# Performance work log

Measured on AMD Instinct MI355X. Metric: run time of the kernel, lower is better.

## Reference

```python
import jax, jax.numpy as jnp
import numpy as np

D_MODEL = 128
NHEAD = 8
DFF = 256
NW = 1024      # number of windows
WIN = 128      # max tokens per window
N_TOTAL = NW * WIN
NEG = -1e9


def _build_indices():
    rng = np.random.RandomState(0)
    cnt = rng.randint(WIN // 2, WIN + 1, size=NW)
    cnt_prv = rng.randint(WIN // 2, WIN + 1, size=NW)
    inds = np.concatenate([w * WIN + np.arange(c) for w, c in enumerate(cnt)]).astype(np.int64)
    inds_prv = np.concatenate([w * WIN + np.arange(c) for w, c in enumerate(cnt_prv)]).astype(np.int64)
    kpm_prv = (np.arange(WIN)[None, :] >= cnt_prv[:, None])  # True = padded key slot
    keep_inds = np.sort(rng.choice(N_TOTAL, len(inds), replace=False)).astype(np.int64)
    keep_inds_prv = np.sort(rng.choice(N_TOTAL, len(inds_prv), replace=False)).astype(np.int64)
    return inds, inds_prv, kpm_prv, keep_inds, keep_inds_prv


def setup_inputs() -> dict:
    inds, inds_prv, kpm_prv, keep_inds, keep_inds_prv = _build_indices()
    key = jax.random.key(0)
    ks = jax.random.split(key, 12)
    f = jnp.float32
    s = 0.05
    d, dff = D_MODEL, DFF
    return {
        'src': jax.random.normal(ks[0], (N_TOTAL, d), f),
        'src_prv': jax.random.normal(ks[1], (N_TOTAL, d), f),
        'pos': jax.random.normal(ks[2], (NW, WIN, d), f),
        'pos_prv': jax.random.normal(ks[3], (NW, WIN, d), f),
        'in_proj_w': jax.random.normal(ks[4], (3 * d, d), f) * s,
        'in_proj_b': jnp.zeros((3 * d,), f),
        'out_proj_w': jax.random.normal(ks[5], (d, d), f) * s,
        'out_proj_b': jnp.zeros((d,), f),
        'lin1_w': jax.random.normal(ks[6], (dff, d), f) * s,
        'lin1_b': jnp.zeros((dff,), f),
        'lin2_w': jax.random.normal(ks[7], (d, dff), f) * s,
        'lin2_b': jnp.zeros((d,), f),
        'ln1_g': jnp.ones((d,), f),
        'ln1_b': jnp.zeros((d,), f),
        'ln2_g': jnp.ones((d,), f),
        'ln2_b': jnp.zeros((d,), f),
        'keep_inds': jnp.asarray(keep_inds),
        'keep_inds_prv': jnp.asarray(keep_inds_prv),
        'inds': jnp.asarray(inds),
        'inds_prv': jnp.asarray(inds_prv),
        'key_padding_mask_prv': jnp.asarray(kpm_prv),
    }


def _layer_norm(x, g, b, eps=1e-5):
    m = x.mean(-1, keepdims=True)
    v = ((x - m) ** 2).mean(-1, keepdims=True)
    return (x - m) / jnp.sqrt(v + eps) * g + b


def reference(src, src_prv, pos, pos_prv, in_proj_w, in_proj_b, out_proj_w, out_proj_b,
              lin1_w, lin1_b, lin2_w, lin2_b, ln1_g, ln1_b, ln2_g, ln2_b,
              keep_inds, keep_inds_prv, inds, inds_prv, key_padding_mask_prv):
    d, h = D_MODEL, NHEAD
    hd = d // h
    # src[keep_inds] gather, then flat2window_v2 scatter into window grid
    sel = src[keep_inds]
    sel_prv = src_prv[keep_inds_prv]
    grid = jnp.zeros((NW * WIN, d), src.dtype).at[inds].set(sel).reshape(NW, WIN, d)
    grid_prv = jnp.zeros((NW * WIN, d), src.dtype).at[inds_prv].set(sel_prv).reshape(NW, WIN, d)
    q = grid + pos
    k = grid_prv + pos_prv
    v = grid_prv
    wq, wk, wv = jnp.split(in_proj_w, 3, axis=0)
    bq, bk, bv = jnp.split(in_proj_b, 3, axis=0)
    qh = (q @ wq.T + bq).reshape(NW, WIN, h, hd)
    kh = (k @ wk.T + bk).reshape(NW, WIN, h, hd)
    vh = (v @ wv.T + bv).reshape(NW, WIN, h, hd)
    scores = jnp.einsum('nqhd,nkhd->nhqk', qh, kh) / np.sqrt(hd).astype(np.float32)
    scores = jnp.where(key_padding_mask_prv[:, None, None, :], NEG, scores)
    attn = jax.nn.softmax(scores, axis=-1)
    out = jnp.einsum('nhqk,nkhd->nqhd', attn, vh).reshape(NW, WIN, d)
    out = out @ out_proj_w.T + out_proj_b
    # window2flat_v2 gather back, residual add at kept positions
    out_sel = out.reshape(NW * WIN, d)[inds]
    src = src.at[keep_inds].add(out_sel)  # dropout1 is identity in eval
    src = _layer_norm(src, ln1_g, ln1_b)
    ff = jax.nn.relu(src @ lin1_w.T + lin1_b) @ lin2_w.T + lin2_b
    src = _layer_norm(src + ff, ln2_g, ln2_b)
    return src
```

## Files before the change

kernel.cpp:

```cpp
#include <hip/hip_runtime.h>

#define NWIN 1024
#define WIN 128
#define DM 128
#define NTOT (NWIN*WIN)

typedef __bf16 bf16;
typedef __bf16 bf16x2 __attribute__((ext_vector_type(2)));
typedef __bf16 bf16x4 __attribute__((ext_vector_type(4)));
typedef __bf16 bf16x8 __attribute__((ext_vector_type(8)));
typedef float f32x4 __attribute__((ext_vector_type(4)));
typedef float f32x16 __attribute__((ext_vector_type(16)));

#define MFMA16(a,b,c) __builtin_amdgcn_mfma_f32_16x16x32_bf16(a,b,c,0,0,0)
#define MFMA32(a,b,c) __builtin_amdgcn_mfma_f32_32x32x16_bf16(a,b,c,0,0,0)

#define QSCALE 0.36067376022224085f


__global__ void k_prep1(const float* __restrict__ inproj, const float* __restrict__ outproj,
                        const float* __restrict__ w1, const float* __restrict__ w2,
                        bf16* __restrict__ whi,
                        int* __restrict__ mq, int* __restrict__ mkv, int* __restrict__ flag) {
    int i = blockIdx.x * 256 + threadIdx.x;
    if (i == 0) *flag = 0;
    float v;
    if (i < 49152)       v = inproj[i];
    else if (i < 65536)  v = outproj[i - 49152];
    else if (i < 98304)  v = w1[i - 65536];
    else                 v = w2[i - 98304];
    if (i < 16384) v *= QSCALE;
    whi[i] = (bf16)v;
    mq[i] = -1; mkv[i] = -1;
}

__global__ void k_prep2(const int* __restrict__ kpm_i, int* __restrict__ flag,
                        const int* __restrict__ inds, const int* __restrict__ keep, int n,
                        const int* __restrict__ inds_p, const int* __restrict__ keep_p, int np,
                        int* __restrict__ mq, int* __restrict__ mkv) {
    int j = blockIdx.x * 256 + threadIdx.x;
    if (j < 32768) {
        int v = kpm_i[j];
        if (v != 0 && v != 1) atomicOr(flag, 1);
    }
    if (j < n)  mq[inds[j]]    = keep[j];
    if (j < np) mkv[inds_p[j]] = keep_p[j];
}

__global__ void k_prep3(const int* __restrict__ kpm_i, const unsigned char* __restrict__ kpm_b,
                        const int* __restrict__ flag, unsigned char* __restrict__ kmask,
                        const float4* __restrict__ s, float4* __restrict__ d, int n4) {
    int i = blockIdx.x * 256 + threadIdx.x;
    if (i < 131072) {
        int byte_mode = *flag;
        kmask[i] = byte_mode ? (kpm_b[i] != 0) : (kpm_i[i] != 0);
    }
    int stride = gridDim.x * 256;
    for (int k = i; k < n4; k += stride) d[k] = s[k];
}

__device__ __forceinline__ void proj1p(const bf16* __restrict__ Xh,
                                       const bf16* __restrict__ WH,
                                       int l15, int g16, f32x4 acc[8]) {
    #pragma unroll
    for (int ks = 0; ks < 4; ks++) {
        bf16x8 ah = *(const bf16x8*)(Xh + l15 * 136 + ks*32 + g16*8);
        #pragma unroll
        for (int tn = 0; tn < 8; tn++) {
            bf16x8 bh = *(const bf16x8*)(WH + (size_t)(16*tn + l15) * DM + ks*32 + g16*8);
            acc[tn] = MFMA16(ah, bh, acc[tn]);
        }
    }
}

__global__ __launch_bounds__(256, 4) void k_qkv(
    const float* __restrict__ src, const float* __restrict__ src_prv,
    const float* __restrict__ pos, const float* __restrict__ pos_prv,
    const bf16* __restrict__ whi,
    const float* __restrict__ bqkv,
    const int* __restrict__ mq, const int* __restrict__ mkv,
    bf16* __restrict__ Qg, bf16* __restrict__ Kg, bf16* __restrict__ Vtg)
{
    const int blk = blockIdx.x;
    const int rbase = blk * 64;
    const int w = blk >> 1;
    const int kb = (blk & 1) * 64;
    const int tid = threadIdx.x;
    const int lane = tid & 63, wv = tid >> 6;
    const int l15 = lane & 15, g16 = lane >> 4;
    __shared__ bf16 Xhi[64*136];
    __shared__ bf16 Bb[9216];

    const int srow = tid >> 2, sq4 = tid & 3;
    const int p = rbase + srow;
    const int gq = mq[p];
    const int gv = mkv[p];

    float4 aq[8], bq[8], vv[8];
    {
        const float4* pr = (const float4*)(pos + (size_t)p * DM + sq4 * 32);
        #pragma unroll
        for (int i = 0; i < 8; i++) aq[i] = pr[i];
        if (gq >= 0) {
            const float4* sr = (const float4*)(src + (size_t)gq * DM + sq4 * 32);
            #pragma unroll
            for (int i = 0; i < 8; i++) bq[i] = sr[i];
        }
        if (gv >= 0) {
            const float4* vr = (const float4*)(src_prv + (size_t)gv * DM + sq4 * 32);
            #pragma unroll
            for (int i = 0; i < 8; i++) vv[i] = vr[i];
        }
        bf16* xh = Xhi + srow * 136 + sq4 * 32;
        #pragma unroll
        for (int i = 0; i < 8; i++) {
            float4 v = aq[i];
            if (gq >= 0) { v.x += bq[i].x; v.y += bq[i].y; v.z += bq[i].z; v.w += bq[i].w; }
            bf16x4 h = { (bf16)v.x, (bf16)v.y, (bf16)v.z, (bf16)v.w };
            *(bf16x4*)(xh + i * 4) = h;
        }
    }
    __syncthreads();

    f32x4 qa[8];
    for (int tn = 0; tn < 8; tn++) qa[tn] = {};
    proj1p(Xhi + 16*wv*136, whi, l15, g16, qa);
    #pragma unroll
    for (int tn = 0; tn < 8; tn++) {
        float bias = bqkv[16*tn + l15] * QSCALE;
        #pragma unroll
        for (int r = 0; r < 4; r++)
            Bb[(16*wv + 4*g16 + r) * 136 + 16*tn + l15] = (bf16)(qa[tn][r] + bias);
    }
    float4 pp[8];
    {
        const float4* ppr = (const float4*)(pos_prv + (size_t)p * DM + sq4 * 32);
        #pragma unroll
        for (int i = 0; i < 8; i++) pp[i] = ppr[i];
    }
    __syncthreads();

    {
        bf16* xh = Xhi + srow * 136 + sq4 * 32;
        if (gv >= 0) {
            #pragma unroll
            for (int i = 0; i < 8; i++) {
                bf16x4 h = { (bf16)vv[i].x, (bf16)vv[i].y, (bf16)vv[i].z, (bf16)vv[i].w };
                *(bf16x4*)(xh + i * 4) = h;
            }
        } else {
            bf16x4 z = { (bf16)0.f, (bf16)0.f, (bf16)0.f, (bf16)0.f };
            #pragma unroll
            for (int i = 0; i < 8; i++) *(bf16x4*)(xh + i * 4) = z;
        }
    }
    #pragma unroll
    for (int it = 0; it < 4; it++) {
        int c = it * 256 + tid;
        int row = c >> 4, off = (c & 15) * 8;
        *(bf16x8*)(Qg + (size_t)(rbase + row) * DM + off) = *(const bf16x8*)(Bb + row*136 + off);
    }
    __syncthreads();

    f32x4 va[8];
    for (int tn = 0; tn < 8; tn++) va[tn] = {};
    proj1p(Xhi + 16*wv*136, whi + 256*DM, l15, g16, va);
    #pragma unroll
    for (int tn = 0; tn < 8; tn++) {
        float bias = bqkv[256 + 16*tn + l15];
        int dim = 16*tn + l15;
        bf16x4 b = { (bf16)(va[tn][0] + bias), (bf16)(va[tn][1] + bias),
                     (bf16)(va[tn][2] + bias), (bf16)(va[tn][3] + bias) };
        *(bf16x4*)(Bb + dim * 72 + 16*wv + 4*g16) = b;
    }
    __syncthreads();

    {
        bf16* xh = Xhi + srow * 136 + sq4 * 32;
        #pragma unroll
        for (int i = 0; i < 8; i++) {
            bf16x4 ch = *(const bf16x4*)(xh + i * 4);
            bf16x4 h = { (bf16)((float)ch.x + pp[i].x), (bf16)((float)ch.y + pp[i].y),
                         (bf16)((float)ch.z + pp[i].z), (bf16)((float)ch.w + pp[i].w) };
            *(bf16x4*)(xh + i * 4) = h;
        }
    }
    #pragma unroll
    for (int it = 0; it < 4; it++) {
        int c = it * 256 + tid;
        int dim = c >> 3, off = (c & 7) * 8;
        *(bf16x8*)(Vtg + ((size_t)w * 128 + dim) * 128 + kb + off) = *(const bf16x8*)(Bb + dim*72 + off);
    }
    __syncthreads();

    f32x4 ka[8];
    for (int tn = 0; tn < 8; tn++) ka[tn] = {};
    proj1p(Xhi + 16*wv*136, whi + 128*DM, l15, g16, ka);
    #pragma unroll
    for (int tn = 0; tn < 8; tn++) {
        float bias = bqkv[128 + 16*tn + l15];
        #pragma unroll
        for (int r = 0; r < 4; r++)
            Bb[(16*wv + 4*g16 + r) * 136 + 16*tn + l15] = (bf16)(ka[tn][r] + bias);
    }
    __syncthreads();
    #pragma unroll
    for (int it = 0; it < 4; it++) {
        int c = it * 256 + tid;
        int row = c >> 4, off = (c & 15) * 8;
        *(bf16x8*)(Kg + (size_t)(rbase + row) * DM + off) = *(const bf16x8*)(Bb + row*136 + off);
    }
}

__global__ __launch_bounds__(256) void k_attn(
    const bf16* __restrict__ Qg, const bf16* __restrict__ Kg, const bf16* __restrict__ Vtg,
    const bf16* __restrict__ whi, const float* __restrict__ ob,
    const unsigned char* __restrict__ kmask, const int* __restrict__ mq,
    float* __restrict__ x1)
{
    const int w = blockIdx.x;
    const int tid = threadIdx.x;
    const int lane = tid & 63, wv = tid >> 6;
    const int l15 = lane & 15, g16 = lane >> 4;
    const int l31 = lane & 31, h32 = lane >> 5;
    __shared__ bf16 P[4][32 * 136];
    bf16* myP = &P[wv][0];

    float mval[4];
    #pragma unroll
    for (int kt = 0; kt < 4; kt++) mval[kt] = kmask[w * WIN + 32*kt + l31] ? -1e9f : 0.f;

    const bf16* Qw = Qg + (size_t)w * WIN * DM;
    const bf16* Kw = Kg + (size_t)w * WIN * DM;
    const bf16* Vw = Vtg + (size_t)w * WIN * DM;

    f32x4 oacc[8][2];
    for (int h = 0; h < 8; h++) { oacc[h][0] = {}; oacc[h][1] = {}; }

    #pragma unroll
    for (int h = 0; h < 8; h++) {
        bf16x8 qf = *(const bf16x8*)(Qw + (size_t)(32*wv + l31) * DM + 16*h + h32*8);
        f32x16 s[4];
        #pragma unroll
        for (int kt = 0; kt < 4; kt++) {
            bf16x8 kf = *(const bf16x8*)(Kw + (size_t)(32*kt + l31) * DM + 16*h + h32*8);
            f32x16 z = {};
            s[kt] = MFMA32(qf, kf, z);
        }
        #pragma unroll
        for (int r = 0; r < 16; r++) {
            float s0 = s[0][r] + mval[0];
            float s1 = s[1][r] + mval[1];
            float s2 = s[2][r] + mval[2];
            float s3 = s[3][r] + mval[3];
            float m = fmaxf(fmaxf(s0, s1), fmaxf(s2, s3));
            #pragma unroll
            for (int d = 1; d <= 16; d <<= 1) m = fmaxf(m, __shfl_xor(m, d));
            float e0 = exp2f(s0 - m), e1 = exp2f(s1 - m);
            float e2 = exp2f(s2 - m), e3 = exp2f(s3 - m);
            float sum = e0 + e1 + e2 + e3;
            #pragma unroll
            for (int d = 1; d <= 16; d <<= 1) sum += __shfl_xor(sum, d);
            float inv = __builtin_amdgcn_rcpf(sum);
            int qrow = (r & 3) + 8 * (r >> 2) + 4 * h32;
            myP[qrow * 136 +      l31] = (bf16)(e0 * inv);
            myP[qrow * 136 + 32 + l31] = (bf16)(e1 * inv);
            myP[qrow * 136 + 64 + l31] = (bf16)(e2 * inv);
            myP[qrow * 136 + 96 + l31] = (bf16)(e3 * inv);
        }
        #pragma unroll
        for (int ks = 0; ks < 4; ks++) {
            bf16x8 p0 = *(const bf16x8*)(myP + (l15     ) * 136 + ks*32 + g16*8);
            bf16x8 p1 = *(const bf16x8*)(myP + (16 + l15) * 136 + ks*32 + g16*8);
            bf16x8 vf = *(const bf16x8*)(Vw + (size_t)(16*h + l15) * DM + ks*32 + g16*8);
            oacc[h][0] = MFMA16(p0, vf, oacc[h][0]);
            oacc[h][1] = MFMA16(p1, vf, oacc[h][1]);
        }
    }

    #pragma unroll
    for (int h = 0; h < 8; h++) {
        #pragma unroll
        for (int tq = 0; tq < 2; tq++) {
            #pragma unroll
            for (int r = 0; r < 4; r++)
                myP[(16*tq + 4*g16 + r) * 136 + 16*h + l15] = (bf16)oacc[h][tq][r];
        }
    }

    const bf16* Woh = whi + 49152;
    f32x4 oc[2][8];
    for (int tq = 0; tq < 2; tq++)
        for (int tn = 0; tn < 8; tn++)
            oc[tq][tn] = {};
    #pragma unroll
    for (int ks = 0; ks < 4; ks++) {
        bf16x8 a0 = *(const bf16x8*)(myP + (l15     ) * 136 + ks*32 + g16*8);
        bf16x8 a1 = *(const bf16x8*)(myP + (16 + l15) * 136 + ks*32 + g16*8);
        #pragma unroll
        for (int tn = 0; tn < 8; tn++) {
            bf16x8 bh = *(const bf16x8*)(Woh + (size_t)(16*tn + l15) * DM + ks*32 + g16*8);
            oc[0][tn] = MFMA16(a0, bh, oc[0][tn]);
            oc[1][tn] = MFMA16(a1, bh, oc[1][tn]);
        }
    }

    float obv[8];
    #pragma unroll
    for (int tn = 0; tn < 8; tn++) obv[tn] = ob[16*tn + l15];
    #pragma unroll
    for (int tq = 0; tq < 2; tq++) {
        #pragma unroll
        for (int r = 0; r < 4; r++) {
            int qrow = 32*wv + 16*tq + 4*g16 + r;
            int g = mq[w * WIN + qrow];
            if (g < 0) continue;
            float* orow = x1 + (size_t)g * DM;
            #pragma unroll
            for (int tn = 0; tn < 8; tn++)
                orow[16*tn + l15] += oc[tq][tn][r] + obv[tn];
        }
    }
}

__global__ __launch_bounds__(256, 4) void k_ffn(
    const float* __restrict__ x1, const bf16* __restrict__ whi,
    const float* __restrict__ g1, const float* __restrict__ b1ln,
    const float* __restrict__ fb1, const float* __restrict__ fb2,
    const float* __restrict__ g2, const float* __restrict__ b2ln,
    float* __restrict__ out)
{
    const int tid = threadIdx.x;
    const int lane = tid & 63, wv = tid >> 6;
    const int l15 = lane & 15, g16 = lane >> 4;
    const int rbase = blockIdx.x * 64 + wv * 16;
    __shared__ bf16 Hb[4][16 * 264];
    bf16* myH = &Hb[wv][0];
    const bf16* W1h = whi + 65536;
    const bf16* W2h = whi + 98304;

    float xv[4][8];
    float sum = 0.f, sq = 0.f;
    const float* xrow = x1 + (size_t)(rbase + l15) * DM;
    #pragma unroll
    for (int ks = 0; ks < 4; ks++) {
        float4 a = *(const float4*)(xrow + ks*32 + g16*8);
        float4 b = *(const float4*)(xrow + ks*32 + g16*8 + 4);
        xv[ks][0]=a.x; xv[ks][1]=a.y; xv[ks][2]=a.z; xv[ks][3]=a.w;
        xv[ks][4]=b.x; xv[ks][5]=b.y; xv[ks][6]=b.z; xv[ks][7]=b.w;
        sum += a.x+a.y+a.z+a.w + b.x+b.y+b.z+b.w;
        sq  += a.x*a.x+a.y*a.y+a.z*a.z+a.w*a.w + b.x*b.x+b.y*b.y+b.z*b.z+b.w*b.w;
    }
    sum += __shfl_xor(sum, 16); sum += __shfl_xor(sum, 32);
    sq  += __shfl_xor(sq, 16);  sq  += __shfl_xor(sq, 32);
    float mean = sum * (1.f/128.f);
    float var  = sq * (1.f/128.f) - mean * mean;
    float rstd = rsqrtf(var + 1e-5f);

    bf16x8 ah[4];
    #pragma unroll
    for (int ks = 0; ks < 4; ks++) {
        #pragma unroll
        for (int j = 0; j < 8; j++) {
            int col = ks*32 + g16*8 + j;
            float y = (xv[ks][j] - mean) * rstd * g1[col] + b1ln[col];
            ah[ks][j] = (bf16)y;
        }
    }

    #pragma unroll
    for (int c = 0; c < 2; c++) {
        f32x4 h1[8];
        #pragma unroll
        for (int t = 0; t < 8; t++) h1[t] = {};
        #pragma unroll
        for (int ks = 0; ks < 4; ks++) {
            #pragma unroll
            for (int t = 0; t < 8; t++) {
                bf16x8 bh = *(const bf16x8*)(W1h + (size_t)(16*(8*c + t) + l15) * DM + ks*32 + g16*8);
                h1[t] = MFMA16(ah[ks], bh, h1[t]);
            }
        }
        #pragma unroll
        for (int t = 0; t < 8; t++) {
            int tn = 8*c + t;
            float bias = fb1[16*tn + l15];
            #pragma unroll
            for (int r = 0; r < 4; r++) {
                float v = fmaxf(h1[t][r] + bias, 0.f);
                myH[(4*g16 + r) * 264 + 16*tn + l15] = (bf16)v;
            }
        }
    }

    f32x4 o[8];
    #pragma unroll
    for (int tn = 0; tn < 8; tn++) o[tn] = {};
    #pragma unroll
    for (int ks = 0; ks < 8; ks++) {
        bf16x8 a = *(const bf16x8*)(myH + l15 * 264 + ks*32 + g16*8);
        #pragma unroll
        for (int tn = 0; tn < 8; tn++) {
            bf16x8 bh = *(const bf16x8*)(W2h + (size_t)(16*tn + l15) * 256 + ks*32 + g16*8);
            o[tn] = MFMA16(a, bh, o[tn]);
        }
    }

    #pragma unroll
    for (int r = 0; r < 4; r++) {
        int rw = 4*g16 + r;
        int row = rbase + rw;
        float bm = __shfl(mean, rw);
        float br = __shfl(rstd, rw);
        float tmp[8];
        float s2 = 0.f, q2 = 0.f;
        #pragma unroll
        for (int tn = 0; tn < 8; tn++) {
            int col = 16*tn + l15;
            float xr = x1[(size_t)row * DM + col];
            float y  = (xr - bm) * br * g1[col] + b1ln[col];
            float v  = o[tn][r] + fb2[col] + y;
            tmp[tn] = v; s2 += v; q2 += v * v;
        }
        #pragma unroll
        for (int d = 1; d <= 8; d <<= 1) { s2 += __shfl_xor(s2, d); q2 += __shfl_xor(q2, d); }
        float mean2 = s2 * (1.f/128.f);
        float var2  = q2 * (1.f/128.f) - mean2 * mean2;
        float rstd2 = rsqrtf(var2 + 1e-5f);
        #pragma unroll
        for (int tn = 0; tn < 8; tn++) {
            int col = 16*tn + l15;
            out[(size_t)row * DM + col] = (tmp[tn] - mean2) * rstd2 * g2[col] + b2ln[col];
        }
    }
}

extern "C" void kernel_launch(void* const* d_in, const int* in_sizes, int n_in,
                              void* d_out, int out_size, void* d_ws, size_t ws_size,
                              hipStream_t stream)
{
    const float* src      = (const float*)d_in[0];
    const float* src_prv  = (const float*)d_in[1];
    const float* pos      = (const float*)d_in[2];
    const float* pos_prv  = (const float*)d_in[3];
    const float* inpw     = (const float*)d_in[4];
    const float* inpb     = (const float*)d_in[5];
    const float* outpw    = (const float*)d_in[6];
    const float* outpb    = (const float*)d_in[7];
    const float* l1w      = (const float*)d_in[8];
    const float* l1b      = (const float*)d_in[9];
    const float* l2w      = (const float*)d_in[10];
    const float* l2b      = (const float*)d_in[11];
    const float* ln1g     = (const float*)d_in[12];
    const float* ln1b     = (const float*)d_in[13];
    const float* ln2g     = (const float*)d_in[14];
    const float* ln2b     = (const float*)d_in[15];
    const int* keep       = (const int*)d_in[16];
    const int* keep_p     = (const int*)d_in[17];
    const int* inds       = (const int*)d_in[18];
    const int* inds_p     = (const int*)d_in[19];
    const int n_inds = in_sizes[18], n_prv = in_sizes[19];

    char* wsb = (char*)d_ws;
    bf16* whi  = (bf16*)(wsb);
    int*  mq   = (int*)(wsb + 524288);
    int*  mkv  = (int*)(wsb + 1048576);
    bf16* Qb   = (bf16*)(wsb + 1572864);
    bf16* Kb   = (bf16*)(wsb + 1572864 + 33554432);
    bf16* Vtb  = (bf16*)(wsb + 1572864 + 2u*33554432);
    unsigned char* kmask = (unsigned char*)(wsb + 1572864 + 3u*33554432);
    int* mflag = (int*)(wsb + 1572864 + 3u*33554432 + 131072);
    float* x1 = (float*)d_out;

    int mmax = n_inds > n_prv ? n_inds : n_prv;
    if (mmax < 32768) mmax = 32768;
    k_prep1<<<512, 256, 0, stream>>>(inpw, outpw, l1w, l2w, whi, mq, mkv, mflag);
    k_prep2<<<(mmax + 255) / 256, 256, 0, stream>>>((const int*)d_in[20], mflag,
                                                    inds, keep, n_inds, inds_p, keep_p, n_prv, mq, mkv);
    k_prep3<<<2048, 256, 0, stream>>>((const int*)d_in[20], (const unsigned char*)d_in[20], mflag, kmask,
                                      (const float4*)src, (float4*)x1, NTOT * DM / 4);
    k_qkv<<<NTOT / 64, 256, 0, stream>>>(src, src_prv, pos, pos_prv, whi, inpb, mq, mkv, Qb, Kb, Vtb);
    k_attn<<<NWIN, 256, 0, stream>>>(Qb, Kb, Vtb, whi, outpb, kmask, mq, x1);
    k_ffn<<<NTOT / 64, 256, 0, stream>>>(x1, whi, ln1g, ln1b, l1b, l2b, ln2g, ln2b, (float*)d_out);
}
```

Measured before the change: 454.4 us.

## Split QKV projection kernel into three role blocks along grid y

The fused QKV kernel, which computed Q, V and K sequentially in one block with several barriers and a reused staging tile, is split so each block computes a single projection selected by blockIdx.y. This triples the grid and removes the serial dependency chain and most syncthreads per block, exposing more parallelism and latency hiding. In exchange, src_prv rows are gathered twice (once for the K role, once for the V role) and the indices are read by more blocks, which adds global memory traffic.

```diff
diff --git a/kernel.cpp b/kernel.cpp
--- a/kernel.cpp
+++ b/kernel.cpp
@@ -82,133 +82,106 @@
     bf16* __restrict__ Qg, bf16* __restrict__ Kg, bf16* __restrict__ Vtg)
 {
     const int blk = blockIdx.x;
+    const int role = blockIdx.y;
     const int rbase = blk * 64;
     const int w = blk >> 1;
     const int kb = (blk & 1) * 64;
     const int tid = threadIdx.x;
     const int lane = tid & 63, wv = tid >> 6;
     const int l15 = lane & 15, g16 = lane >> 4;
-    __shared__ bf16 Xhi[64*136];
+    __shared__ bf16 X[64*136];
     __shared__ bf16 Bb[9216];
 
     const int srow = tid >> 2, sq4 = tid & 3;
     const int p = rbase + srow;
-    const int gq = mq[p];
-    const int gv = mkv[p];
-
-    float4 aq[8], bq[8], vv[8];
-    {
+
+    if (role == 0) {
+        const int g = mq[p];
+        float4 a[8];
         const float4* pr = (const float4*)(pos + (size_t)p * DM + sq4 * 32);
         #pragma unroll
-        for (int i = 0; i < 8; i++) aq[i] = pr[i];
-        if (gq >= 0) {
-            const float4* sr = (const float4*)(src + (size_t)gq * DM + sq4 * 32);
-            #pragma unroll
-            for (int i = 0; i < 8; i++) bq[i] = sr[i];
-        }
-        if (gv >= 0) {
-            const float4* vr = (const float4*)(src_prv + (size_t)gv * DM + sq4 * 32);
-            #pragma unroll
-            for (int i = 0; i < 8; i++) vv[i] = vr[i];
-        }
-        bf16* xh = Xhi + srow * 136 + sq4 * 32;
+        for (int i = 0; i < 8; i++) a[i] = pr[i];
+        if (g >= 0) {
+            const float4* sr = (const float4*)(src + (size_t)g * DM + sq4 * 32);
+            #pragma unroll
+            for (int i = 0; i < 8; i++) {
+                float4 s4 = sr[i];
+                a[i].x += s4.x; a[i].y += s4.y; a[i].z += s4.z; a[i].w += s4.w;
+            }
+        }
+        bf16* xh = X + srow * 136 + sq4 * 32;
         #pragma unroll
         for (int i = 0; i < 8; i++) {
-            float4 v = aq[i];
-            if (gq >= 0) { v.x += bq[i].x; v.y += bq[i].y; v.z += bq[i].z; v.w += bq[i].w; }
-            bf16x4 h = { (bf16)v.x, (bf16)v.y, (bf16)v.z, (bf16)v.w };
+            bf16x4 h = { (bf16)a[i].x, (bf16)a[i].y, (bf16)a[i].z, (bf16)a[i].w };
             *(bf16x4*)(xh + i * 4) = h;
         }
+    } else {
+        const int g = mkv[p];
+        float4 a[8];
+        if (role == 2) {
+            const float4* pr = (const float4*)(pos_prv + (size_t)p * DM + sq4 * 32);
+            #pragma unroll
+            for (int i = 0; i < 8; i++) a[i] = pr[i];
+        } else {
+            #pragma unroll
+            for (int i = 0; i < 8; i++) a[i] = make_float4(0.f, 0.f, 0.f, 0.f);
+        }
+        if (g >= 0) {
+            const float4* sr = (const float4*)(src_prv + (size_t)g * DM + sq4 * 32);
+            #pragma unroll
+            for (int i = 0; i < 8; i++) {
+                float4 s4 = sr[i];
+                a[i].x += s4.x; a[i].y += s4.y; a[i].z += s4.z; a[i].w += s4.w;
+            }
+        }
+        bf16* xh = X + srow * 136 + sq4 * 32;
+        #pragma unroll
+        for (int i = 0; i < 8; i++) {
+            bf16x4 h = { (bf16)a[i].x, (bf16)a[i].y, (bf16)a[i].z, (bf16)a[i].w };
+            *(bf16x4*)(xh + i * 4) = h;
+        }
     }
     __syncthreads();
 
-    f32x4 qa[8];
-    for (int tn = 0; tn < 8; tn++) qa[tn] = {};
-    proj1p(Xhi + 16*wv*136, whi, l15, g16, qa);
-    #pragma unroll
-    for (int tn = 0; tn < 8; tn++) {
-        float bias = bqkv[16*tn + l15] * QSCALE;
-        #pragma unroll
-        for (int r = 0; r < 4; r++)
-            Bb[(16*wv + 4*g16 + r) * 136 + 16*tn + l15] = (bf16)(qa[tn][r] + bias);
-    }
-    float4 pp[8];
-    {
-        const float4* ppr = (const float4*)(pos_prv + (size_t)p * DM + sq4 * 32);
-        #pragma unroll
-        for (int i = 0; i < 8; i++) pp[i] = ppr[i];
-    }
-    __syncthreads();
-
-    {
-        bf16* xh = Xhi + srow * 136 + sq4 * 32;
-        if (gv >= 0) {
-            #pragma unroll
-            for (int i = 0; i < 8; i++) {
-                bf16x4 h = { (bf16)vv[i].x, (bf16)vv[i].y, (bf16)vv[i].z, (bf16)vv[i].w };
-                *(bf16x4*)(xh + i * 4) = h;
-            }
-        } else {
-            bf16x4 z = { (bf16)0.f, (bf16)0.f, (bf16)0.f, (bf16)0.f };
-            #pragma unroll
-            for (int i = 0; i < 8; i++) *(bf16x4*)(xh + i * 4) = z;
-        }
-    }
-    #pragma unroll
-    for (int it = 0; it < 4; it++) {
-        int c = it * 256 + tid;
-        int row = c >> 4, off = (c & 15) * 8;
-        *(bf16x8*)(Qg + (size_t)(rbase + row) * DM + off) = *(const bf16x8*)(Bb + row*136 + off);
-    }
-    __syncthreads();
-
-    f32x4 va[8];
-    for (int tn = 0; tn < 8; tn++) va[tn] = {};
-    proj1p(Xhi + 16*wv*136, whi + 256*DM, l15, g16, va);
-    #pragma unroll
-    for (int tn = 0; tn < 8; tn++) {
-        float bias = bqkv[256 + 16*tn + l15];
-        int dim = 16*tn + l15;
-        bf16x4 b = { (bf16)(va[tn][0] + bias), (bf16)(va[tn][1] + bias),
-                     (bf16)(va[tn][2] + bias), (bf16)(va[tn][3] + bias) };
-        *(bf16x4*)(Bb + dim * 72 + 16*wv + 4*g16) = b;
-    }
-    __syncthreads();
-
-    {
-        bf16* xh = Xhi + srow * 136 + sq4 * 32;
-        #pragma unroll
-        for (int i = 0; i < 8; i++) {
-            bf16x4 ch = *(const bf16x4*)(xh + i * 4);
-            bf16x4 h = { (bf16)((float)ch.x + pp[i].x), (bf16)((float)ch.y + pp[i].y),
-                         (bf16)((float)ch.z + pp[i].z), (bf16)((float)ch.w + pp[i].w) };
-            *(bf16x4*)(xh + i * 4) = h;
-        }
-    }
-    #pragma unroll
-    for (int it = 0; it < 4; it++) {
-        int c = it * 256 + tid;
-        int dim = c >> 3, off = (c & 7) * 8;
-        *(bf16x8*)(Vtg + ((size_t)w * 128 + dim) * 128 + kb + off) = *(const bf16x8*)(Bb + dim*72 + off);
-    }
-    __syncthreads();
-
-    f32x4 ka[8];
-    for (int tn = 0; tn < 8; tn++) ka[tn] = {};
-    proj1p(Xhi + 16*wv*136, whi + 128*DM, l15, g16, ka);
-    #pragma unroll
-    for (int tn = 0; tn < 8; tn++) {
-        float bias = bqkv[128 + 16*tn + l15];
-        #pragma unroll
-        for (int r = 0; r < 4; r++)
-            Bb[(16*wv + 4*g16 + r) * 136 + 16*tn + l15] = (bf16)(ka[tn][r] + bias);
-    }
-    __syncthreads();
-    #pragma unroll
-    for (int it = 0; it < 4; it++) {
-        int c = it * 256 + tid;
-        int row = c >> 4, off = (c & 15) * 8;
-        *(bf16x8*)(Kg + (size_t)(rbase + row) * DM + off) = *(const bf16x8*)(Bb + row*136 + off);
+    const bf16* W = whi + (role == 0 ? 0 : (role == 1 ? 256*DM : 128*DM));
+    f32x4 acc[8];
+    for (int tn = 0; tn < 8; tn++) acc[tn] = {};
+    proj1p(X + 16*wv*136, W, l15, g16, acc);
+
+    if (role == 1) {
+        #pragma unroll
+        for (int tn = 0; tn < 8; tn++) {
+            float bias = bqkv[256 + 16*tn + l15];
+            int dim = 16*tn + l15;
+            bf16x4 b = { (bf16)(acc[tn][0] + bias), (bf16)(acc[tn][1] + bias),
+                         (bf16)(acc[tn][2] + bias), (bf16)(acc[tn][3] + bias) };
+            *(bf16x4*)(Bb + dim * 72 + 16*wv + 4*g16) = b;
+        }
+        __syncthreads();
+        #pragma unroll
+        for (int it = 0; it < 4; it++) {
+            int c = it * 256 + tid;
+            int dim = c >> 3, off = (c & 7) * 8;
+            *(bf16x8*)(Vtg + ((size_t)w * 128 + dim) * 128 + kb + off) = *(const bf16x8*)(Bb + dim*72 + off);
+        }
+    } else {
+        const float bsc  = (role == 0) ? QSCALE : 1.f;
+        const int   boff = (role == 0) ? 0 : 128;
+        #pragma unroll
+        for (int tn = 0; tn < 8; tn++) {
+            float bias = bqkv[boff + 16*tn + l15] * bsc;
+            #pragma unroll
+            for (int r = 0; r < 4; r++)
+                Bb[(16*wv + 4*g16 + r) * 136 + 16*tn + l15] = (bf16)(acc[tn][r] + bias);
+        }
+        __syncthreads();
+        bf16* dst = (role == 0) ? Qg : Kg;
+        #pragma unroll
+        for (int it = 0; it < 4; it++) {
+            int c = it * 256 + tid;
+            int row = c >> 4, off = (c & 15) * 8;
+            *(bf16x8*)(dst + (size_t)(rbase + row) * DM + off) = *(const bf16x8*)(Bb + row*136 + off);
+        }
     }
 }
 
@@ -479,7 +452,7 @@
                                                     inds, keep, n_inds, inds_p, keep_p, n_prv, mq, mkv);
     k_prep3<<<2048, 256, 0, stream>>>((const int*)d_in[20], (const unsigned char*)d_in[20], mflag, kmask,
                                       (const float4*)src, (float4*)x1, NTOT * DM / 4);
-    k_qkv<<<NTOT / 64, 256, 0, stream>>>(src, src_prv, pos, pos_prv, whi, inpb, mq, mkv, Qb, Kb, Vtb);
+    k_qkv<<<dim3(2048, 3), 256, 0, stream>>>(src, src_prv, pos, pos_prv, whi, inpb, mq, mkv, Qb, Kb, Vtb);
     k_attn<<<NWIN, 256, 0, stream>>>(Qb, Kb, Vtb, whi, outpb, kmask, mq, x1);
     k_ffn<<<NTOT / 64, 256, 0, stream>>>(x1, whi, ln1g, ln1b, l1b, l2b, ln2g, ln2b, (float*)d_out);
 }
```

Result: no change. 456.0 us (+0.3%).
